# Performance work log

Measured on AMD Instinct MI355X. Metric: run time of the kernel, lower is better.

Reference implementation:

```python
import jax, jax.numpy as jnp
import numpy as np

N, E, G = 20000, 320000, 128
D, H, C, L = 128, 8, 16, 4  # hidden, heads, per-head dim, layers
F_NODE, F_EDGE, T = 9, 3, 10


def _lin_init(key, fan_in, shape):
    return jax.random.normal(key, shape, dtype=jnp.float32) / np.sqrt(fan_in)


def setup_inputs() -> dict:
    key = jax.random.key(0)
    ks = jax.random.split(key, 24)
    inp = {
        "x": jax.random.normal(ks[0], (N, F_NODE), dtype=jnp.float32),
        "edge_index": jax.random.randint(ks[1], (2, E), 0, N),
        "edge_attr": jax.random.normal(ks[2], (E, F_EDGE), dtype=jnp.float32),
        "batch": jnp.sort(jax.random.randint(ks[3], (N,), 0, G)),
        # encoders
        "node_w": _lin_init(ks[4], F_NODE, (F_NODE, D)), "node_b": jnp.zeros((D,), jnp.float32),
        "edge_w": _lin_init(ks[5], F_EDGE, (F_EDGE, D)), "edge_b": jnp.zeros((D,), jnp.float32),
        # per-layer TransformerConv params (stacked over L)
        "Wq": _lin_init(ks[6], D, (L, D, D)), "bq": jnp.zeros((L, D), jnp.float32),
        "Wk": _lin_init(ks[7], D, (L, D, D)), "bk": jnp.zeros((L, D), jnp.float32),
        "Wv": _lin_init(ks[8], D, (L, D, D)), "bv": jnp.zeros((L, D), jnp.float32),
        "We": _lin_init(ks[9], D, (L, D, D)),  # lin_edge (no bias in PyG)
        "Wskip": _lin_init(ks[10], D, (L, D, D)), "bskip": jnp.zeros((L, D), jnp.float32),
        "Wbeta": _lin_init(ks[11], 3 * D, (L, 3 * D)),  # lin_beta (no bias)
        "ln_g": jnp.ones((L, D), jnp.float32), "ln_b": jnp.zeros((L, D), jnp.float32),
        # prediction head
        "h1_w": _lin_init(ks[12], D, (D, D // 2)), "h1_b": jnp.zeros((D // 2,), jnp.float32),
        "h2_w": _lin_init(ks[13], D // 2, (D // 2, T)), "h2_b": jnp.zeros((T,), jnp.float32),
    }
    return inp


def _layer_norm(x, g, b, eps=1e-5):
    mu = jnp.mean(x, -1, keepdims=True)
    var = jnp.mean(jnp.square(x - mu), -1, keepdims=True)
    return (x - mu) * jax.lax.rsqrt(var + eps) * g + b


def _transformer_conv(h, ea, src, dst, Wq, bq, Wk, bk, Wv, bv, We, Wskip, bskip, Wbeta):
    # PyG TransformerConv, concat=True, beta=True, edge_dim=D, eval mode (no dropout)
    q = (h @ Wq + bq)[dst].reshape(E, H, C)           # query at destination i
    k = (h @ Wk + bk)[src].reshape(E, H, C)
    v = (h @ Wv + bv)[src].reshape(E, H, C)
    e = (ea @ We).reshape(E, H, C)
    k = k + e
    alpha = jnp.sum(q * k, -1) / np.sqrt(C)           # [E, H]
    m = jax.ops.segment_max(alpha, dst, num_segments=N)
    alpha = jnp.exp(alpha - m[dst])
    denom = jax.ops.segment_sum(alpha, dst, num_segments=N)
    alpha = alpha / (denom[dst] + 1e-16)
    msg = (v + e) * alpha[..., None]                  # [E, H, C]
    out = jax.ops.segment_sum(msg, dst, num_segments=N).reshape(N, D)
    x_r = h @ Wskip + bskip                           # root/skip transform
    beta = jax.nn.sigmoid(jnp.concatenate([out, x_r, out - x_r], -1) @ Wbeta)  # [N]
    return beta[:, None] * x_r + (1.0 - beta)[:, None] * out


def reference(x, edge_index, edge_attr, batch, node_w, node_b, edge_w, edge_b,
              Wq, bq, Wk, bk, Wv, bv, We, Wskip, bskip, Wbeta, ln_g, ln_b,
              h1_w, h1_b, h2_w, h2_b):
    src, dst = edge_index[0], edge_index[1]
    h = jax.nn.relu(x @ node_w + node_b)              # node encoder + relu
    ea = edge_attr @ edge_w + edge_b                  # edge encoder
    for l in range(L):
        h_res = h
        h = _transformer_conv(h, ea, src, dst, Wq[l], bq[l], Wk[l], bk[l],
                              Wv[l], bv[l], We[l], Wskip[l], bskip[l], Wbeta[l])
        h = _layer_norm(h + h_res, ln_g[l], ln_b[l])
    # global mean pool over graphs
    sums = jax.ops.segment_sum(h, batch, num_segments=G)
    cnt = jax.ops.segment_sum(jnp.ones((N,), h.dtype), batch, num_segments=G)
    pooled = sums / jnp.maximum(cnt, 1.0)[:, None]    # [G, D]
    return jax.nn.relu(pooled @ h1_w + h1_b) @ h2_w + h2_b  # [G, T]
```

## Files before the change

### kernel.cpp

```cpp
#include <hip/hip_runtime.h>
#include <hip/hip_bf16.h>

typedef __hip_bfloat16 bf16;
typedef __attribute__((ext_vector_type(8))) short short8;
typedef __attribute__((ext_vector_type(4))) float f32x4;

#define DEV __device__ __forceinline__

DEV float blo(unsigned u) { return __uint_as_float(u << 16); }
DEV float bhi(unsigned u) { return __uint_as_float(u & 0xffff0000u); }

DEV float waveReduceSum(float v) {
#pragma unroll
    for (int m = 1; m < 64; m <<= 1) v += __shfl_xor(v, m);
    return v;
}

DEV float red8(float v) {
    v += __shfl_xor(v, 8);
    v += __shfl_xor(v, 16);
    v += __shfl_xor(v, 32);
    return v;
}

__global__ __launch_bounds__(256) void pack_w_k(
    const float* __restrict__ Wq, const float* __restrict__ Wk,
    const float* __restrict__ Wv, const float* __restrict__ Ws,
    bf16* __restrict__ outp, int L) {
    int t = blockIdx.x * 256 + threadIdx.x;
    if (t >= 4 * L * 16384) return;
    int p = t & 16383;
    int ls = t >> 14;
    int l = ls >> 2, s = ls & 3;
    int j = p & 7, ln = (p >> 3) & 63, kb = (p >> 9) & 3, nb = p >> 11;
    int k = kb * 32 + (ln >> 4) * 8 + j;
    int n = nb * 16 + (ln & 15);
    const float* W = (s == 0) ? Wq : (s == 1) ? Wk : (s == 2) ? Wv : Ws;
    outp[t] = __float2bfloat16(W[(size_t)l * 16384 + k * 128 + n]);
}

__global__ __launch_bounds__(256) void pack_b_k(
    const float* __restrict__ bq, const float* __restrict__ bk,
    const float* __restrict__ bv, const float* __restrict__ bs,
    float* __restrict__ outp, int L) {
    int t = blockIdx.x * 256 + threadIdx.x;
    if (t >= 4 * L * 128) return;
    int d = t & 127;
    int ls = t >> 7;
    int l = ls >> 2, s = ls & 3;
    const float* B = (s == 0) ? bq : (s == 1) ? bk : (s == 2) ? bv : bs;
    outp[t] = B[l * 128 + d];
}

__global__ __launch_bounds__(256) void edge_mats_k(
    const float* __restrict__ edge_w, const float* __restrict__ edge_b,
    const float* __restrict__ We, float* __restrict__ Me, int L) {
    int t = blockIdx.x * 256 + threadIdx.x;
    if (t >= L * 4 * 128) return;
    int n = t & 127, j = (t >> 7) & 3, l = t >> 9;
    const float* W = We + (size_t)l * 16384;
    const float* row = (j < 3) ? (edge_w + j * 128) : edge_b;
    float acc = 0.f;
    for (int d = 0; d < 128; ++d) acc += row[d] * W[d * 128 + n];
    Me[t] = acc;
}

__global__ __launch_bounds__(256) void hist_k(const int* __restrict__ ei,
                                              int* __restrict__ deg, int E) {
    int e = blockIdx.x * 256 + threadIdx.x;
    if (e >= E) return;
    atomicAdd(&deg[ei[E + e]], 1);
}

__global__ __launch_bounds__(1024) void scan_k(const int* __restrict__ deg,
                                               int* __restrict__ off,
                                               int* __restrict__ cursor, int N, int E) {
    __shared__ int part[1024];
    int t = threadIdx.x;
    int chunk = (N + 1023) >> 10;
    int lo = t * chunk, hi = min(lo + chunk, N);
    int s = 0;
    for (int i = lo; i < hi; ++i) s += deg[i];
    part[t] = s;
    __syncthreads();
    for (int d = 1; d < 1024; d <<= 1) {
        int v = (t >= d) ? part[t - d] : 0;
        __syncthreads();
        part[t] += v;
        __syncthreads();
    }
    int base = (t == 0) ? 0 : part[t - 1];
    for (int i = lo; i < hi; ++i) {
        off[i] = base;
        cursor[i] = base;
        base += deg[i];
    }
    if (t == 1023) off[N] = E;
}

__global__ __launch_bounds__(256) void fill_k(const int* __restrict__ ei,
                                              const float* __restrict__ eattr,
                                              int* __restrict__ cursor,
                                              int* __restrict__ el_src,
                                              float4* __restrict__ ea4, int E) {
    int e = blockIdx.x * 256 + threadIdx.x;
    if (e >= E) return;
    int dst = ei[E + e];
    int pos = atomicAdd(&cursor[dst], 1);
    el_src[pos] = ei[e];
    ea4[pos] = make_float4(eattr[e * 3], eattr[e * 3 + 1], eattr[e * 3 + 2], 0.f);
}

__global__ __launch_bounds__(256) void node_enc_k(
    const float* __restrict__ x, const float* __restrict__ w,
    const float* __restrict__ b, float* __restrict__ h,
    bf16* __restrict__ h_bf, int N) {
    int t = blockIdx.x * 256 + threadIdx.x;
    if (t >= N * 128) return;
    int n = t >> 7, d = t & 127;
    float acc = b[d];
#pragma unroll
    for (int i = 0; i < 9; ++i) acc += x[n * 9 + i] * w[i * 128 + d];
    float r = fmaxf(acc, 0.f);
    h[t] = r;
    h_bf[t] = __float2bfloat16(r);
}

__global__ __launch_bounds__(256) void qkvs_k(
    const bf16* __restrict__ A, const bf16* __restrict__ Wp,
    const float* __restrict__ bp,
    bf16* __restrict__ Q, bf16* __restrict__ kv,
    float* __restrict__ S, int M) {
    int tid = threadIdx.x;
    int l = tid & 63, w = tid >> 6;
    int row0 = blockIdx.x * 64;
    const short* Ab = (const short*)A + (size_t)(row0 + (l & 15)) * 128 + ((l >> 4) * 8);
    short8 a[4][4];
#pragma unroll
    for (int mb = 0; mb < 4; ++mb)
#pragma unroll
        for (int kb = 0; kb < 4; ++kb)
            a[mb][kb] = *(const short8*)(Ab + mb * 16 * 128 + kb * 32);
    int colb = w * 32 + (l & 15);
#pragma unroll
    for (int s = 0; s < 4; ++s) {
        const short* Wb = (const short*)Wp + s * 16384;
        short8 bfr[2][4];
#pragma unroll
        for (int nbi = 0; nbi < 2; ++nbi)
#pragma unroll
            for (int kb = 0; kb < 4; ++kb)
                bfr[nbi][kb] = *(const short8*)(Wb + (size_t)(((w * 2 + nbi) * 4 + kb) * 64 + l) * 8);
        f32x4 acc[4][2] = {};
#pragma unroll
        for (int kb = 0; kb < 4; ++kb)
#pragma unroll
            for (int mb = 0; mb < 4; ++mb)
#pragma unroll
                for (int nbi = 0; nbi < 2; ++nbi)
                    acc[mb][nbi] = __builtin_amdgcn_mfma_f32_16x16x32_bf16(
                        a[mb][kb], bfr[nbi][kb], acc[mb][nbi], 0, 0, 0);
        float bias0 = bp[s * 128 + colb];
        float bias1 = bp[s * 128 + colb + 16];
#pragma unroll
        for (int mb = 0; mb < 4; ++mb) {
            int rbase = row0 + mb * 16 + (l >> 4) * 4;
#pragma unroll
            for (int j = 0; j < 4; ++j) {
                int r = rbase + j;
                if (r >= M) continue;
#pragma unroll
                for (int nbi = 0; nbi < 2; ++nbi) {
                    int c = colb + nbi * 16;
                    float v = acc[mb][nbi][j] + (nbi ? bias1 : bias0);
                    if (s == 0) {
                        Q[(size_t)r * 128 + c] = __float2bfloat16(v);
                    } else if (s == 3) {
                        S[(size_t)r * 128 + c] = v;
                    } else {
                        kv[(size_t)r * 256 + ((s == 2) ? 128 : 0) + c] = __float2bfloat16(v);
                    }
                }
            }
        }
    }
}

__global__ __launch_bounds__(256) void qm_k(
    const bf16* __restrict__ Q, const float* __restrict__ Me,
    float4* __restrict__ qm, int N) {
    int t = blockIdx.x * 256 + threadIdx.x;
    if (t >= N * 8) return;
    int n = t >> 3, hh = t & 7;
    const unsigned* qr = (const unsigned*)Q + (size_t)n * 64 + hh * 8;
    unsigned qq[8];
    *(uint4*)&qq[0] = *(const uint4*)qr;
    *(uint4*)&qq[4] = *(const uint4*)(qr + 4);
    float a0 = 0.f, a1 = 0.f, a2 = 0.f, a3 = 0.f;
#pragma unroll
    for (int k = 0; k < 8; ++k) {
        float x0 = blo(qq[k]), x1 = bhi(qq[k]);
        int d = hh * 16 + 2 * k;
        a0 += x0 * Me[d]       + x1 * Me[d + 1];
        a1 += x0 * Me[128 + d] + x1 * Me[128 + d + 1];
        a2 += x0 * Me[256 + d] + x1 * Me[256 + d + 1];
        a3 += x0 * Me[384 + d] + x1 * Me[384 + d + 1];
    }
    qm[t] = make_float4(a0, a1, a2, a3);
}

__global__ __launch_bounds__(256) void attn_k(
    const int* __restrict__ off, const int* __restrict__ el_src,
    const float4* __restrict__ ea4, const float* __restrict__ Me,
    const float4* __restrict__ qm, const bf16* __restrict__ Q,
    const bf16* __restrict__ kv, const float* __restrict__ S,
    float* __restrict__ h, bf16* __restrict__ h_bf,
    const float* __restrict__ Wb, const float* __restrict__ lng,
    const float* __restrict__ lnb, int N) {
    int gw = (blockIdx.x * 256 + threadIdx.x) >> 6;
    int l = threadIdx.x & 63;
    int nw = (gridDim.x * 256) >> 6;
    int hh = l & 7, sl = l >> 3;
    int d0 = hh * 16 + sl * 2, d1 = d0 + 1;
    float me00 = Me[d0],       me01 = Me[d1];
    float me10 = Me[128 + d0], me11 = Me[128 + d1];
    float me20 = Me[256 + d0], me21 = Me[256 + d1];
    float me30 = Me[384 + d0], me31 = Me[384 + d1];
    float wba0 = Wb[d0],       wba1 = Wb[d1];
    float wbb0 = Wb[128 + d0], wbb1 = Wb[128 + d1];
    float wbc0 = Wb[256 + d0], wbc1 = Wb[256 + d1];
    float g0 = lng[d0], g1 = lng[d1];
    float bb0 = lnb[d0], bb1 = lnb[d1];
    for (int n = gw; n < N; n += nw) {
        const unsigned* qr = (const unsigned*)Q + (size_t)n * 64 + hh * 8;
        unsigned qq[8];
        *(uint4*)&qq[0] = *(const uint4*)qr;
        *(uint4*)&qq[4] = *(const uint4*)(qr + 4);
        float q[16];
#pragma unroll
        for (int k = 0; k < 8; ++k) { q[2 * k] = blo(qq[k]); q[2 * k + 1] = bhi(qq[k]); }
        float4 qmv = qm[(size_t)n * 8 + hh];
        float acc[16] = {};
        float S0 = 0.f, S1 = 0.f, S2 = 0.f, den = 0.f;
        int i0 = off[n], i1 = off[n + 1];
        int nit = (i1 - i0 + 7) >> 3;
        for (int it = 0; it < nit; ++it) {
            int idx = i0 + it * 8 + sl;
            bool ok = idx < i1;
            int ci = ok ? idx : (i1 - 1);
            int src = el_src[ci];
            float4 ae = ea4[ci];
            const unsigned* kr = (const unsigned*)kv + (size_t)src * 128 + hh * 8;
            unsigned kk[8], vv[8];
            *(uint4*)&kk[0] = *(const uint4*)kr;
            *(uint4*)&kk[4] = *(const uint4*)(kr + 4);
            *(uint4*)&vv[0] = *(const uint4*)(kr + 64);
            *(uint4*)&vv[4] = *(const uint4*)(kr + 68);
            float sd = fmaf(ae.x, qmv.x, fmaf(ae.y, qmv.y, fmaf(ae.z, qmv.z, qmv.w)));
#pragma unroll
            for (int k = 0; k < 8; ++k)
                sd = fmaf(q[2 * k], blo(kk[k]), fmaf(q[2 * k + 1], bhi(kk[k]), sd));
            float p = ok ? __expf(sd * 0.25f) : 0.f;
            den += p;
            S0 = fmaf(p, ae.x, S0);
            S1 = fmaf(p, ae.y, S1);
            S2 = fmaf(p, ae.z, S2);
#pragma unroll
            for (int k = 0; k < 8; ++k) {
                acc[2 * k]     = fmaf(p, blo(vv[k]), acc[2 * k]);
                acc[2 * k + 1] = fmaf(p, bhi(vv[k]), acc[2 * k + 1]);
            }
        }
        den = red8(den); S0 = red8(S0); S1 = red8(S1); S2 = red8(S2);
#pragma unroll
        for (int k = 0; k < 16; ++k) acc[k] = red8(acc[k]);
        float inv = den > 0.f ? 1.f / den : 0.f;
        float o0 = (acc[sl * 2]     + S0 * me00 + S1 * me10 + S2 * me20 + den * me30) * inv;
        float o1 = (acc[sl * 2 + 1] + S0 * me01 + S1 * me11 + S2 * me21 + den * me31) * inv;
        size_t base = (size_t)n * 128;
        float s0 = S[base + d0], s1 = S[base + d1];
        float part = o0 * wba0 + s0 * wbb0 + (o0 - s0) * wbc0
                   + o1 * wba1 + s1 * wbb1 + (o1 - s1) * wbc1;
        float g = waveReduceSum(part);
        float beta = 1.f / (1.f + __expf(-g));
        float y0 = beta * s0 + (1.f - beta) * o0;
        float y1 = beta * s1 + (1.f - beta) * o1;
        float z0 = y0 + h[base + d0];
        float z1 = y1 + h[base + d1];
        float mean = waveReduceSum(z0 + z1) * (1.f / 128.f);
        float c0 = z0 - mean, c1 = z1 - mean;
        float var = waveReduceSum(c0 * c0 + c1 * c1) * (1.f / 128.f);
        float invs = rsqrtf(var + 1e-5f);
        float r0 = c0 * invs * g0 + bb0;
        float r1 = c1 * invs * g1 + bb1;
        h[base + d0] = r0;
        h[base + d1] = r1;
        h_bf[base + d0] = __float2bfloat16(r0);
        h_bf[base + d1] = __float2bfloat16(r1);
    }
}

__global__ __launch_bounds__(256) void pool_partial_k(
    const float* __restrict__ h, const int* __restrict__ batch,
    float* __restrict__ psum, int N) {
    int d = threadIdx.x & 127;
    int half = threadIdx.x >> 7;
    int n0 = blockIdx.x * 64;
    int n1 = min(n0 + 64, N);
    float acc = 0.f;
    int curg = -1;
    for (int n = n0 + half; n < n1; n += 2) {
        int g = batch[n];
        if (g != curg) {
            if (curg >= 0) atomicAdd(&psum[curg * 128 + d], acc);
            acc = 0.f;
            curg = g;
        }
        acc += h[(size_t)n * 128 + d];
    }
    if (curg >= 0) atomicAdd(&psum[curg * 128 + d], acc);
}

__global__ __launch_bounds__(128) void head2_k(
    const float* __restrict__ psum, const int* __restrict__ batch,
    const float* __restrict__ h1w, const float* __restrict__ h1b,
    const float* __restrict__ h2w, const float* __restrict__ h2b,
    float* __restrict__ out, int N) {
    int g = blockIdx.x;
    int t = threadIdx.x;
    auto lb = [&](int val) {
        int lo = 0, hi = N;
        while (lo < hi) {
            int mid = (lo + hi) >> 1;
            if (batch[mid] < val) lo = mid + 1; else hi = mid;
        }
        return lo;
    };
    int s = lb(g), e = lb(g + 1);
    float cnt = fmaxf((float)(e - s), 1.f);
    __shared__ float pl[128];
    __shared__ float hid[64];
    pl[t] = psum[g * 128 + t] / cnt;
    __syncthreads();
    if (t < 64) {
        float a = h1b[t];
        for (int k = 0; k < 128; ++k) a += pl[k] * h1w[k * 64 + t];
        hid[t] = fmaxf(a, 0.f);
    }
    __syncthreads();
    if (t < 10) {
        float o = h2b[t];
        for (int k = 0; k < 64; ++k) o += hid[k] * h2w[k * 10 + t];
        out[g * 10 + t] = o;
    }
}

extern "C" void kernel_launch(void* const* d_in, const int* in_sizes, int n_in,
                              void* d_out, int out_size, void* d_ws, size_t ws_size,
                              hipStream_t stream) {
    const float* x      = (const float*)d_in[0];
    const int*   ei     = (const int*)d_in[1];
    const float* eattr  = (const float*)d_in[2];
    const int*   batch  = (const int*)d_in[3];
    const float* node_w = (const float*)d_in[4];
    const float* node_b = (const float*)d_in[5];
    const float* edge_w = (const float*)d_in[6];
    const float* edge_b = (const float*)d_in[7];
    const float* Wq     = (const float*)d_in[8];
    const float* bq     = (const float*)d_in[9];
    const float* Wk     = (const float*)d_in[10];
    const float* bk     = (const float*)d_in[11];
    const float* Wv     = (const float*)d_in[12];
    const float* bv     = (const float*)d_in[13];
    const float* We     = (const float*)d_in[14];
    const float* Wskip  = (const float*)d_in[15];
    const float* bskip  = (const float*)d_in[16];
    const float* Wbeta  = (const float*)d_in[17];
    const float* ln_g   = (const float*)d_in[18];
    const float* ln_b   = (const float*)d_in[19];
    const float* h1_w   = (const float*)d_in[20];
    const float* h1_b   = (const float*)d_in[21];
    const float* h2_w   = (const float*)d_in[22];
    const float* h2_b   = (const float*)d_in[23];
    float* out = (float*)d_out;

    const int N = in_sizes[3];
    const int E = in_sizes[2] / 3;
    const int L = in_sizes[8] / 16384;
    const int G = out_size / 10;

    char* wptr = (char*)d_ws;
    auto alloc = [&](size_t bytes) {
        char* p = wptr;
        wptr += (bytes + 255) & ~(size_t)255;
        return p;
    };
    float* h      = (float*)alloc((size_t)(N + 64) * 128 * 4);
    bf16*  h_bf   = (bf16*)alloc((size_t)(N + 64) * 128 * 2);
    bf16*  Qb     = (bf16*)alloc((size_t)(N + 64) * 128 * 2);
    bf16*  kv     = (bf16*)alloc((size_t)(N + 64) * 256 * 2);
    float* S      = (float*)alloc((size_t)(N + 64) * 128 * 4);
    float4* qm    = (float4*)alloc((size_t)N * 8 * 16);
    float4* ea4   = (float4*)alloc((size_t)E * 16);
    bf16*  Wpack  = (bf16*)alloc((size_t)4 * L * 16384 * 2);
    float* bpack  = (float*)alloc((size_t)4 * L * 128 * 4);
    float* Me     = (float*)alloc((size_t)L * 4 * 128 * 4);
    int*   deg    = (int*)alloc((size_t)N * 4);
    int*   off    = (int*)alloc((size_t)(N + 1) * 4);
    int*   cursor = (int*)alloc((size_t)N * 4);
    int*   el_src = (int*)alloc((size_t)E * 4);
    float* psum   = (float*)alloc((size_t)G * 128 * 4);

    dim3 b256(256), b128(128);

    pack_w_k<<<(4 * L * 16384 + 255) / 256, b256, 0, stream>>>(Wq, Wk, Wv, Wskip, Wpack, L);
    pack_b_k<<<(4 * L * 128 + 255) / 256, b256, 0, stream>>>(bq, bk, bv, bskip, bpack, L);
    edge_mats_k<<<(L * 4 * 128 + 255) / 256, b256, 0, stream>>>(edge_w, edge_b, We, Me, L);
    hipMemsetAsync(deg, 0, (size_t)N * 4, stream);
    hist_k<<<(E + 255) / 256, b256, 0, stream>>>(ei, deg, E);
    scan_k<<<1, 1024, 0, stream>>>(deg, off, cursor, N, E);
    fill_k<<<(E + 255) / 256, b256, 0, stream>>>(ei, eattr, cursor, el_src, ea4, E);
    node_enc_k<<<(N * 128 + 255) / 256, b256, 0, stream>>>(x, node_w, node_b, h, h_bf, N);

    int gN = (N + 63) / 64;
    int gAttn = (N + 3) / 4;
    int gQm = (N * 8 + 255) / 256;
    for (int l = 0; l < L; ++l) {
        const float* Me_l = Me + (size_t)l * 512;
        qkvs_k<<<gN, b256, 0, stream>>>(h_bf, Wpack + (size_t)l * 4 * 16384,
                                        bpack + (size_t)l * 4 * 128, Qb, kv, S, N);
        qm_k<<<gQm, b256, 0, stream>>>(Qb, Me_l, qm, N);
        attn_k<<<gAttn, b256, 0, stream>>>(off, el_src, ea4, Me_l, qm,
                                           Qb, kv, S, h, h_bf,
                                           Wbeta + (size_t)l * 384,
                                           ln_g + (size_t)l * 128, ln_b + (size_t)l * 128, N);
    }

    hipMemsetAsync(psum, 0, (size_t)G * 128 * 4, stream);
    pool_partial_k<<<gN, b256, 0, stream>>>(h, batch, psum, N);
    head2_k<<<G, b128, 0, stream>>>(psum, batch, h1_w, h1_b, h2_w, h2_b, out, N);
}
```

Measured before the change: 378.2 us.

## Fuse qm computation into attention kernel and prefetch next edge batch

Drops the separate qm_k kernel and computes each head's query-edge projection (q·Me) inside the attention kernel, removing one launch per layer and the qm buffer round trip. The edge loop is also software-pipelined: the next batch's source index, edge attributes and K/V rows are loaded while the current batch is processed, to hide gather latency. The cost is more registers per thread (a second set of kk/vv/ae), which may lower occupancy.

```diff
diff --git a/kernel.cpp b/kernel.cpp
--- a/kernel.cpp
+++ b/kernel.cpp
@@ -186,34 +186,11 @@
     }
 }
 
-__global__ __launch_bounds__(256) void qm_k(
-    const bf16* __restrict__ Q, const float* __restrict__ Me,
-    float4* __restrict__ qm, int N) {
-    int t = blockIdx.x * 256 + threadIdx.x;
-    if (t >= N * 8) return;
-    int n = t >> 3, hh = t & 7;
-    const unsigned* qr = (const unsigned*)Q + (size_t)n * 64 + hh * 8;
-    unsigned qq[8];
-    *(uint4*)&qq[0] = *(const uint4*)qr;
-    *(uint4*)&qq[4] = *(const uint4*)(qr + 4);
-    float a0 = 0.f, a1 = 0.f, a2 = 0.f, a3 = 0.f;
-#pragma unroll
-    for (int k = 0; k < 8; ++k) {
-        float x0 = blo(qq[k]), x1 = bhi(qq[k]);
-        int d = hh * 16 + 2 * k;
-        a0 += x0 * Me[d]       + x1 * Me[d + 1];
-        a1 += x0 * Me[128 + d] + x1 * Me[128 + d + 1];
-        a2 += x0 * Me[256 + d] + x1 * Me[256 + d + 1];
-        a3 += x0 * Me[384 + d] + x1 * Me[384 + d + 1];
-    }
-    qm[t] = make_float4(a0, a1, a2, a3);
-}
-
 __global__ __launch_bounds__(256) void attn_k(
     const int* __restrict__ off, const int* __restrict__ el_src,
     const float4* __restrict__ ea4, const float* __restrict__ Me,
-    const float4* __restrict__ qm, const bf16* __restrict__ Q,
-    const bf16* __restrict__ kv, const float* __restrict__ S,
+    const bf16* __restrict__ Q, const bf16* __restrict__ kv,
+    const float* __restrict__ S,
     float* __restrict__ h, bf16* __restrict__ h_bf,
     const float* __restrict__ Wb, const float* __restrict__ lng,
     const float* __restrict__ lnb, int N) {
@@ -239,24 +216,54 @@
         float q[16];
 #pragma unroll
         for (int k = 0; k < 8; ++k) { q[2 * k] = blo(qq[k]); q[2 * k + 1] = bhi(qq[k]); }
-        float4 qmv = qm[(size_t)n * 8 + hh];
+        float qm0 = 0.f, qm1 = 0.f, qm2 = 0.f, qm3 = 0.f;
+#pragma unroll
+        for (int c = 0; c < 4; ++c) {
+            float4 r0 = *(const float4*)(Me + hh * 16 + c * 4);
+            float4 r1 = *(const float4*)(Me + 128 + hh * 16 + c * 4);
+            float4 r2 = *(const float4*)(Me + 256 + hh * 16 + c * 4);
+            float4 r3 = *(const float4*)(Me + 384 + hh * 16 + c * 4);
+            qm0 += q[c*4]*r0.x + q[c*4+1]*r0.y + q[c*4+2]*r0.z + q[c*4+3]*r0.w;
+            qm1 += q[c*4]*r1.x + q[c*4+1]*r1.y + q[c*4+2]*r1.z + q[c*4+3]*r1.w;
+            qm2 += q[c*4]*r2.x + q[c*4+1]*r2.y + q[c*4+2]*r2.z + q[c*4+3]*r2.w;
+            qm3 += q[c*4]*r3.x + q[c*4+1]*r3.y + q[c*4+2]*r3.z + q[c*4+3]*r3.w;
+        }
         float acc[16] = {};
         float S0 = 0.f, S1 = 0.f, S2 = 0.f, den = 0.f;
         int i0 = off[n], i1 = off[n + 1];
         int nit = (i1 - i0 + 7) >> 3;
-        for (int it = 0; it < nit; ++it) {
-            int idx = i0 + it * 8 + sl;
-            bool ok = idx < i1;
-            int ci = ok ? idx : (i1 - 1);
+        unsigned kk[8], vv[8];
+        float4 ae = make_float4(0, 0, 0, 0);
+        bool ok = false;
+        if (nit > 0) {
+            int idx = i0 + sl;
+            ok = idx < i1;
+            int ci = ok ? idx : 0;
             int src = el_src[ci];
-            float4 ae = ea4[ci];
+            ae = ea4[ci];
             const unsigned* kr = (const unsigned*)kv + (size_t)src * 128 + hh * 8;
-            unsigned kk[8], vv[8];
             *(uint4*)&kk[0] = *(const uint4*)kr;
             *(uint4*)&kk[4] = *(const uint4*)(kr + 4);
             *(uint4*)&vv[0] = *(const uint4*)(kr + 64);
             *(uint4*)&vv[4] = *(const uint4*)(kr + 68);
-            float sd = fmaf(ae.x, qmv.x, fmaf(ae.y, qmv.y, fmaf(ae.z, qmv.z, qmv.w)));
+        }
+        for (int it = 0; it < nit; ++it) {
+            unsigned kk2[8] = {}, vv2[8] = {};
+            float4 ae2 = make_float4(0, 0, 0, 0);
+            bool ok2 = false;
+            if (it + 1 < nit) {
+                int idx2 = i0 + (it + 1) * 8 + sl;
+                ok2 = idx2 < i1;
+                int ci2 = ok2 ? idx2 : 0;
+                int src2 = el_src[ci2];
+                ae2 = ea4[ci2];
+                const unsigned* kr2 = (const unsigned*)kv + (size_t)src2 * 128 + hh * 8;
+                *(uint4*)&kk2[0] = *(const uint4*)kr2;
+                *(uint4*)&kk2[4] = *(const uint4*)(kr2 + 4);
+                *(uint4*)&vv2[0] = *(const uint4*)(kr2 + 64);
+                *(uint4*)&vv2[4] = *(const uint4*)(kr2 + 68);
+            }
+            float sd = fmaf(ae.x, qm0, fmaf(ae.y, qm1, fmaf(ae.z, qm2, qm3)));
 #pragma unroll
             for (int k = 0; k < 8; ++k)
                 sd = fmaf(q[2 * k], blo(kk[k]), fmaf(q[2 * k + 1], bhi(kk[k]), sd));
@@ -270,6 +277,10 @@
                 acc[2 * k]     = fmaf(p, blo(vv[k]), acc[2 * k]);
                 acc[2 * k + 1] = fmaf(p, bhi(vv[k]), acc[2 * k + 1]);
             }
+#pragma unroll
+            for (int k = 0; k < 8; ++k) { kk[k] = kk2[k]; vv[k] = vv2[k]; }
+            ae = ae2;
+            ok = ok2;
         }
         den = red8(den); S0 = red8(S0); S1 = red8(S1); S2 = red8(S2);
 #pragma unroll
@@ -400,7 +411,6 @@
     bf16*  Qb     = (bf16*)alloc((size_t)(N + 64) * 128 * 2);
     bf16*  kv     = (bf16*)alloc((size_t)(N + 64) * 256 * 2);
     float* S      = (float*)alloc((size_t)(N + 64) * 128 * 4);
-    float4* qm    = (float4*)alloc((size_t)N * 8 * 16);
     float4* ea4   = (float4*)alloc((size_t)E * 16);
     bf16*  Wpack  = (bf16*)alloc((size_t)4 * L * 16384 * 2);
     float* bpack  = (float*)alloc((size_t)4 * L * 128 * 4);
@@ -424,13 +434,11 @@
 
     int gN = (N + 63) / 64;
     int gAttn = (N + 3) / 4;
-    int gQm = (N * 8 + 255) / 256;
     for (int l = 0; l < L; ++l) {
         const float* Me_l = Me + (size_t)l * 512;
         qkvs_k<<<gN, b256, 0, stream>>>(h_bf, Wpack + (size_t)l * 4 * 16384,
                                         bpack + (size_t)l * 4 * 128, Qb, kv, S, N);
-        qm_k<<<gQm, b256, 0, stream>>>(Qb, Me_l, qm, N);
-        attn_k<<<gAttn, b256, 0, stream>>>(off, el_src, ea4, Me_l, qm,
+        attn_k<<<gAttn, b256, 0, stream>>>(off, el_src, ea4, Me_l,
                                            Qb, kv, S, h, h_bf,
                                            Wbeta + (size_t)l * 384,
                                            ln_g + (size_t)l * 128, ln_b + (size_t)l * 128, N);
```

Result: slower. 482.5 us (+27.6%).
